# Optimization experiments

Hardware: AMD Instinct MI355X
Metric: run time of the kernel (lower is better)

Reference implementation:

```python
import jax, jax.numpy as jnp
import numpy as np


def setup_inputs() -> dict:
    key = jax.random.key(0)
    B, T, D, H = 32, 1600, 512, 512
    # variable lengths, nonincreasing (PackedSequence convention)
    lengths = np.array([T - 25 * i for i in range(B)])            # 1600 .. 825
    bs = (lengths[None, :] > np.arange(T)[:, None]).sum(1)        # batch_sizes[t], nonincreasing
    t_idx = np.repeat(np.arange(T), bs)                           # packed element -> timestep
    b_idx = np.concatenate([np.arange(b) for b in bs])            # packed element -> batch row
    mask = np.arange(B)[None, :] < bs[:, None]                    # [T,B] active mask
    total = int(bs.sum())                                         # 38800
    ks = jax.random.split(key, 7)
    s = 1.0 / np.sqrt(H)
    return {
        "packed_data": jax.random.normal(ks[0], (total, D), jnp.float32),
        "h0": jax.random.normal(ks[1], (B, H), jnp.float32),
        "c0": jax.random.normal(ks[2], (B, H), jnp.float32),
        "w_ih": jax.random.uniform(ks[3], (4 * H, D), jnp.float32, -s, s),
        "w_hh": jax.random.uniform(ks[4], (4 * H, H), jnp.float32, -s, s),
        "b_ih": jax.random.uniform(ks[5], (4 * H,), jnp.float32, -s, s),
        "b_hh": jax.random.uniform(ks[6], (4 * H,), jnp.float32, -s, s),
        "t_idx": jnp.asarray(t_idx, jnp.int32),
        "b_idx": jnp.asarray(b_idx, jnp.int32),
        "mask": jnp.asarray(mask),
    }


def reference(packed_data, h0, c0, w_ih, w_hh, b_ih, b_hh, t_idx, b_idx, mask):
    # Reverse LSTM over a packed variable-length batch.
    # Equivalent math to the torch loop: process timesteps T-1 .. 0; a row's
    # hidden stays at its initial value until the row becomes active.
    T, B = mask.shape
    D = packed_data.shape[1]
    # unpack to padded [T,B,D] (zeros at inactive slots; never read for output)
    padded = jnp.zeros((T, B, D), packed_data.dtype).at[t_idx, b_idx].set(packed_data)

    def step(carry, xm):
        h, c = carry
        x, m = xm                                   # x:[B,D], m:[B]
        gates = x @ w_ih.T + b_ih + h @ w_hh.T + b_hh   # [B,4H]
        i, f, g, o = jnp.split(gates, 4, axis=-1)
        c_new = jax.nn.sigmoid(f) * c + jax.nn.sigmoid(i) * jnp.tanh(g)
        h_new = jax.nn.sigmoid(o) * jnp.tanh(c_new)
        m2 = m[:, None]
        # inactive rows keep their initial hidden until they enter the batch
        return (jnp.where(m2, h_new, h0), jnp.where(m2, c_new, c0)), h_new

    (hT, cT), outs = jax.lax.scan(step, (h0, c0), (padded[::-1], mask[::-1]))
    outs = outs[::-1]                               # [T,B,H], time-forward order
    packed_out = outs[t_idx, b_idx]                 # repack [total,H]
    return packed_out, hT, cT
```

## Files before the change

### kernel.cpp

```cpp
#include <hip/hip_runtime.h>
#include <hip/hip_bf16.h>
#include <stdint.h>

typedef __attribute__((ext_vector_type(8))) short bf16x8;
typedef __attribute__((ext_vector_type(4))) float f32x4;
typedef __attribute__((ext_vector_type(4))) int int4v;
typedef unsigned long long u64;

#define DD 512
#define HH 512
#define BB 32

__device__ __forceinline__ unsigned short f2bf(float f) {
  unsigned u = __float_as_uint(f);
  u += 0x7fffu + ((u >> 16) & 1u);
  return (unsigned short)(u >> 16);
}
__device__ __forceinline__ int pk2(float a, float b) {
  return (int)((unsigned)f2bf(a) | ((unsigned)f2bf(b) << 16));
}
__device__ __forceinline__ float sigf(float x) { return 1.f / (1.f + __expf(-x)); }
__device__ __forceinline__ float tanhfast(float x) {
  float e = __expf(fminf(fmaxf(2.f * x, -60.f), 60.f));
  return (e - 1.f) / (e + 1.f);
}

__global__ void init_state(u64* hbuf, const float* __restrict__ h0, int* L) {
  int i = blockIdx.x * blockDim.x + threadIdx.x;
  if (i < 32) L[i] = 0;
  if (i < 16384) {
    int g = i >> 13, p = (i >> 12) & 1, m = (i >> 8) & 15, q = i & 255;
    u64 v;
    if (p == 0) {
      int b = g * 16 + m;
      unsigned lo = f2bf(h0[(size_t)b * HH + 2 * q]);
      unsigned hi = f2bf(h0[(size_t)b * HH + 2 * q + 1]);
      v = (u64)(lo | (hi << 16));
    } else {
      v = 0xFFFFFFFF00000000ull;
    }
    hbuf[i] = v;
  }
}

__global__ void init_idx(const int* __restrict__ t_idx, const int* __restrict__ b_idx,
                         int* rowstart, int* L, int total) {
  int r = blockIdx.x * blockDim.x + threadIdx.x;
  if (r >= total) return;
  int t = t_idx[r];
  if (r == 0 || t_idx[r - 1] != t) rowstart[t] = r;
  atomicMax(&L[b_idx[r]], t + 1);
}

__global__ __launch_bounds__(512, 2)
void lstm_main(const float* __restrict__ X, const float* __restrict__ h0,
               const float* __restrict__ c0, const float* __restrict__ w_ih,
               const float* __restrict__ w_hh, const float* __restrict__ b_ih,
               const float* __restrict__ b_hh, const int* __restrict__ rowstart,
               const int* __restrict__ L, u64* hbuf,
               float* out, int total)
{
  const int tid = threadIdx.x;
  const int bid = blockIdx.x;
  const int g = bid & 1;
  const int k = bid >> 1;
  const int lane = tid & 63;
  const int wave = tid >> 6;
  const int gate = wave & 3;
  const int cs = wave >> 2;
  const int ul = lane & 15;
  const int kc = lane >> 4;
  const int u0 = k * 32;
  const int j = gate * 512 + u0 + cs * 16 + ul;

  __shared__ unsigned short h_st[16 * DD];
  __shared__ unsigned short x_st[16 * DD];
  __shared__ float gl[4][16][32];

  bf16x8 wfa[16], wfb[16];
#pragma unroll
  for (int kk = 0; kk < 16; kk++) {
    const float* pa = w_ih + (size_t)j * DD + kk * 32 + kc * 8;
    const float* pb = w_hh + (size_t)j * DD + kk * 32 + kc * 8;
    bf16x8 va, vb;
#pragma unroll
    for (int e = 0; e < 8; e++) { va[e] = (short)f2bf(pa[e]); vb[e] = (short)f2bf(pb[e]); }
    wfa[kk] = va; wfb[kk] = vb;
  }
  const float bias = b_ih[j] + b_hh[j];

  const int mC = tid >> 5;
  const int uC = tid & 31;
  const int bcell = g * 16 + mC;
  const int Lc = L[bcell];
  float c_reg = c0[(size_t)bcell * HH + u0 + uC];
  const float c0c = c_reg;
  const float h0c = h0[(size_t)bcell * HH + u0 + uC];

  int t0 = 0;
#pragma unroll
  for (int m = 0; m < 16; m++) t0 = max(t0, L[g * 16 + m]);
  t0 -= 1;
  const int S = t0 + 1;

  u64* hb_g = hbuf + g * 8192;
  const size_t hT_off = (size_t)total * HH;
  const size_t cT_off = hT_off + (size_t)BB * HH;

  char* hst_c = (char*)h_st;
  char* xst_c = (char*)x_st;
  const int gr = (mC + k) & 15;
  const int gc = (uC + 2 * k) & 31;
  const int hbyte = gr * 1024 + gc * 32, hsw = (gr & 7) << 4;
  const int xbyte = mC * 1024 + uC * 32, xsw = (mC & 7) << 4;
  const int arow = ul * 1024, aswz = (ul & 7) << 4;

  f32x4 xr[4];
  {
    if (t0 < Lc) {
      const f32x4* xp = (const f32x4*)(X + (size_t)(rowstart[t0] + bcell) * DD + uC * 16);
#pragma unroll
      for (int q = 0; q < 4; q++) xr[q] = xp[q];
    } else {
#pragma unroll
      for (int q = 0; q < 4; q++) xr[q] = (f32x4){0.f, 0.f, 0.f, 0.f};
    }
  }

  for (int s = 0, t = t0; s < S; s++, t--) {
    const bool act = (t < Lc);
    {
      int4v e0 = {pk2(xr[0][0], xr[0][1]), pk2(xr[0][2], xr[0][3]),
                  pk2(xr[1][0], xr[1][1]), pk2(xr[1][2], xr[1][3])};
      int4v e1 = {pk2(xr[2][0], xr[2][1]), pk2(xr[2][2], xr[2][3]),
                  pk2(xr[3][0], xr[3][1]), pk2(xr[3][2], xr[3][3])};
      *(int4v*)(xst_c + (xbyte ^ xsw)) = e0;
      *(int4v*)(xst_c + ((xbyte + 16) ^ xsw)) = e1;
    }
    __syncthreads();

    const u64* src = hb_g + (size_t)((s & 1) * 4096) + gr * 256 + gc * 8;
    int4v c0v, c1v, c2v, c3v;
    asm volatile(
      "global_load_dwordx4 %0, %4, off sc0 sc1\n\t"
      "global_load_dwordx4 %1, %5, off sc0 sc1\n\t"
      "global_load_dwordx4 %2, %6, off sc0 sc1\n\t"
      "global_load_dwordx4 %3, %7, off sc0 sc1"
      : "=&v"(c0v), "=&v"(c1v), "=&v"(c2v), "=&v"(c3v)
      : "v"(src), "v"(src + 2), "v"(src + 4), "v"(src + 6)
      : "memory");

    f32x4 C = {bias, bias, bias, bias};
#pragma unroll
    for (int kk = 0; kk < 16; kk++) {
      bf16x8 A = *(const bf16x8*)(xst_c + ((arow + kk * 64 + kc * 16) ^ aswz));
      C = __builtin_amdgcn_mfma_f32_16x16x32_bf16(A, wfa[kk], C, 0, 0, 0);
    }

    asm volatile("s_waitcnt vmcnt(0)" ::: "memory");
    __builtin_amdgcn_sched_barrier(0);
    const unsigned want = (unsigned)s;
    int spins = 0;
    while (!(((unsigned)c0v[1] == want) & ((unsigned)c0v[3] == want) &
             ((unsigned)c1v[1] == want) & ((unsigned)c1v[3] == want) &
             ((unsigned)c2v[1] == want) & ((unsigned)c2v[3] == want) &
             ((unsigned)c3v[1] == want) & ((unsigned)c3v[3] == want))) {
      if (++spins < 4096) {
        asm volatile(
          "global_load_dwordx4 %0, %4, off sc0 sc1\n\t"
          "global_load_dwordx4 %1, %5, off sc0 sc1\n\t"
          "global_load_dwordx4 %2, %6, off sc0 sc1\n\t"
          "global_load_dwordx4 %3, %7, off sc0 sc1\n\t"
          "s_waitcnt vmcnt(0)"
          : "=&v"(c0v), "=&v"(c1v), "=&v"(c2v), "=&v"(c3v)
          : "v"(src), "v"(src + 2), "v"(src + 4), "v"(src + 6)
          : "memory");
        __builtin_amdgcn_sched_barrier(0);
      } else {
        u64 a0 = __hip_atomic_load(src + 0, __ATOMIC_RELAXED, __HIP_MEMORY_SCOPE_AGENT);
        u64 a1 = __hip_atomic_load(src + 1, __ATOMIC_RELAXED, __HIP_MEMORY_SCOPE_AGENT);
        u64 a2 = __hip_atomic_load(src + 2, __ATOMIC_RELAXED, __HIP_MEMORY_SCOPE_AGENT);
        u64 a3 = __hip_atomic_load(src + 3, __ATOMIC_RELAXED, __HIP_MEMORY_SCOPE_AGENT);
        u64 a4 = __hip_atomic_load(src + 4, __ATOMIC_RELAXED, __HIP_MEMORY_SCOPE_AGENT);
        u64 a5 = __hip_atomic_load(src + 5, __ATOMIC_RELAXED, __HIP_MEMORY_SCOPE_AGENT);
        u64 a6 = __hip_atomic_load(src + 6, __ATOMIC_RELAXED, __HIP_MEMORY_SCOPE_AGENT);
        u64 a7 = __hip_atomic_load(src + 7, __ATOMIC_RELAXED, __HIP_MEMORY_SCOPE_AGENT);
        c0v = (int4v){(int)a0, (int)(a0 >> 32), (int)a1, (int)(a1 >> 32)};
        c1v = (int4v){(int)a2, (int)(a2 >> 32), (int)a3, (int)(a3 >> 32)};
        c2v = (int4v){(int)a4, (int)(a4 >> 32), (int)a5, (int)(a5 >> 32)};
        c3v = (int4v){(int)a6, (int)(a6 >> 32), (int)a7, (int)(a7 >> 32)};
      }
    }

    {
      bool nact = false;
      if (t > 0) {
        nact = ((t - 1) < Lc);
        if (nact) {
          const f32x4* xp = (const f32x4*)(X + (size_t)(rowstart[t - 1] + bcell) * DD + uC * 16);
#pragma unroll
          for (int q = 0; q < 4; q++) xr[q] = xp[q];
        }
      }
      if (!nact) {
#pragma unroll
        for (int q = 0; q < 4; q++) xr[q] = (f32x4){0.f, 0.f, 0.f, 0.f};
      }
    }

    {
      int4v d0 = {c0v[0], c0v[2], c1v[0], c1v[2]};
      int4v d1 = {c2v[0], c2v[2], c3v[0], c3v[2]};
      *(int4v*)(hst_c + (hbyte ^ hsw)) = d0;
      *(int4v*)(hst_c + ((hbyte + 16) ^ hsw)) = d1;
    }
    __syncthreads();

    f32x4 C2 = {0.f, 0.f, 0.f, 0.f};
#pragma unroll
    for (int kk = 0; kk < 8; kk++) {
      bf16x8 A0 = *(const bf16x8*)(hst_c + ((arow + (2 * kk) * 64 + kc * 16) ^ aswz));
      bf16x8 A1 = *(const bf16x8*)(hst_c + ((arow + (2 * kk + 1) * 64 + kc * 16) ^ aswz));
      C  = __builtin_amdgcn_mfma_f32_16x16x32_bf16(A0, wfb[2 * kk], C, 0, 0, 0);
      C2 = __builtin_amdgcn_mfma_f32_16x16x32_bf16(A1, wfb[2 * kk + 1], C2, 0, 0, 0);
    }
#pragma unroll
    for (int r = 0; r < 4; r++) C[r] += C2[r];

#pragma unroll
    for (int r = 0; r < 4; r++) gl[gate][kc * 4 + r][cs * 16 + ul] = C[r];
    __syncthreads();

    float gi = gl[0][mC][uC], gf = gl[1][mC][uC], gg = gl[2][mC][uC], go = gl[3][mC][uC];
    float iv = sigf(gi), fv = sigf(gf), gv = tanhfast(gg), ov = sigf(go);
    float cn = fv * c_reg + iv * gv;
    float hn = ov * tanhfast(cn);
    float hp = act ? hn : h0c;
    c_reg = act ? cn : c0c;

    {
      unsigned hbf = (unsigned)f2bf(hp);
      unsigned v1 = __shfl_down(hbf, 1);
      if ((uC & 1) == 0) {
        u64 val = ((u64)(unsigned)(s + 1) << 32) | (hbf & 0xffffu) | ((v1 & 0xffffu) << 16);
        u64* dst = hb_g + (size_t)(((s + 1) & 1) * 4096) + mC * 256 + k * 16 + (uC >> 1);
        __hip_atomic_store(dst, val, __ATOMIC_RELAXED, __HIP_MEMORY_SCOPE_AGENT);
      }
    }

    if (act) {
      const int rst = rowstart[t];
      out[(size_t)(rst + bcell) * HH + u0 + uC] = hn;
      if (t == 0) {
        out[hT_off + (size_t)bcell * HH + u0 + uC] = hn;
        out[cT_off + (size_t)bcell * HH + u0 + uC] = cn;
      }
    }
  }
}

extern "C" void kernel_launch(void* const* d_in, const int* in_sizes, int n_in,
                              void* d_out, int out_size, void* d_ws, size_t ws_size,
                              hipStream_t stream) {
  const float* X    = (const float*)d_in[0];
  const float* h0   = (const float*)d_in[1];
  const float* c0   = (const float*)d_in[2];
  const float* w_ih = (const float*)d_in[3];
  const float* w_hh = (const float*)d_in[4];
  const float* b_ih = (const float*)d_in[5];
  const float* b_hh = (const float*)d_in[6];
  const int* t_idx  = (const int*)d_in[7];
  const int* b_idx  = (const int*)d_in[8];
  int total = in_sizes[0] / DD;

  u64* hbuf     = (u64*)d_ws;
  int* rowstart = (int*)((char*)d_ws + 131072);
  int* L        = rowstart + 2048;

  hipLaunchKernelGGL(init_state, dim3(64), dim3(256), 0, stream, hbuf, h0, L);
  hipLaunchKernelGGL(init_idx, dim3((total + 255) / 256), dim3(256), 0, stream,
                     t_idx, b_idx, rowstart, L, total);
  hipLaunchKernelGGL(lstm_main, dim3(32), dim3(512), 0, stream,
                     X, h0, c0, w_ih, w_hh, b_ih, b_hh, rowstart, L, hbuf,
                     (float*)d_out, total);
}
```

Measured before the change: 4.521 ms.

## Precompute input projection with a parallel GEMM before the recurrent loop

Adds a standalone bf16 MFMA GEMM that computes X·W_ih^T plus both biases for all packed rows up front and stores the result as bf16 in the workspace. The recurrent kernel then only does the h·W_hh product per step and adds the precomputed gate inputs, which removes the x staging, a barrier and 16 MFMAs from the serial critical path. It also splits the recurrent accumulation into two chains and pads the gate scratch array. The cost is an extra kernel plus about 160 MB of bf16 writes and reads, and extra rounding of the input contribution. The old fused kernel is kept as a fallback when the workspace is too small.

```diff
diff --git a/kernel.cpp b/kernel.cpp
--- a/kernel.cpp
+++ b/kernel.cpp
@@ -18,6 +18,9 @@
 }
 __device__ __forceinline__ int pk2(float a, float b) {
   return (int)((unsigned)f2bf(a) | ((unsigned)f2bf(b) << 16));
+}
+__device__ __forceinline__ float bf2f(unsigned short v) {
+  return __uint_as_float((unsigned)v << 16);
 }
 __device__ __forceinline__ float sigf(float x) { return 1.f / (1.f + __expf(-x)); }
 __device__ __forceinline__ float tanhfast(float x) {
@@ -52,13 +55,100 @@
   atomicMax(&L[b_idx[r]], t + 1);
 }
 
+__global__ __launch_bounds__(256, 2)
+void gx_gemm(const float* __restrict__ X, const float* __restrict__ w_ih,
+             const float* __restrict__ b_ih, const float* __restrict__ b_hh,
+             unsigned short* __restrict__ GX, int total)
+{
+  const int ct = blockIdx.x & 7;
+  const int rt = blockIdx.x >> 3;
+  const int r0 = rt * 64;
+  const int j0 = ct * 256;
+  const int tid = threadIdx.x;
+  const int lane = tid & 63, wv = tid >> 6;
+  const int ul = lane & 15, kc = lane >> 4;
+
+  __shared__ unsigned short As[64 * 64];
+  __shared__ unsigned short Bs[256 * 64];
+  char* As_c = (char*)As;
+  char* Bs_c = (char*)Bs;
+
+  f32x4 acc[4][4];
+#pragma unroll
+  for (int mf = 0; mf < 4; mf++)
+#pragma unroll
+    for (int nf = 0; nf < 4; nf++) acc[mf][nf] = (f32x4){0.f, 0.f, 0.f, 0.f};
+
+  const int arow_s = tid >> 2;
+  const int akq = (tid & 3) * 16;
+  const size_t arow_g = (size_t)min(r0 + arow_s, total - 1);
+  const int ab = arow_s * 128 + akq * 2, asw = (arow_s & 7) << 4;
+  const int bcol = tid;
+  const int bb = bcol * 128, bsw = (bcol & 7) << 4;
+
+  for (int ch = 0; ch < 8; ch++) {
+    const int k0 = ch * 64;
+    {
+      const f32x4* ap = (const f32x4*)(X + arow_g * DD + k0 + akq);
+      f32x4 a0 = ap[0], a1 = ap[1], a2 = ap[2], a3 = ap[3];
+      int4v p0 = {pk2(a0[0], a0[1]), pk2(a0[2], a0[3]), pk2(a1[0], a1[1]), pk2(a1[2], a1[3])};
+      int4v p1 = {pk2(a2[0], a2[1]), pk2(a2[2], a2[3]), pk2(a3[0], a3[1]), pk2(a3[2], a3[3])};
+      *(int4v*)(As_c + (ab ^ asw)) = p0;
+      *(int4v*)(As_c + ((ab + 16) ^ asw)) = p1;
+    }
+    {
+      const f32x4* bp = (const f32x4*)(w_ih + (size_t)(j0 + bcol) * DD + k0);
+#pragma unroll
+      for (int q = 0; q < 4; q++) {
+        f32x4 b0 = bp[4 * q], b1 = bp[4 * q + 1], b2 = bp[4 * q + 2], b3 = bp[4 * q + 3];
+        int4v p0 = {pk2(b0[0], b0[1]), pk2(b0[2], b0[3]), pk2(b1[0], b1[1]), pk2(b1[2], b1[3])};
+        int4v p1 = {pk2(b2[0], b2[1]), pk2(b2[2], b2[3]), pk2(b3[0], b3[1]), pk2(b3[2], b3[3])};
+        *(int4v*)(Bs_c + ((bb + q * 32) ^ bsw)) = p0;
+        *(int4v*)(Bs_c + ((bb + q * 32 + 16) ^ bsw)) = p1;
+      }
+    }
+    __syncthreads();
+#pragma unroll
+    for (int ks = 0; ks < 2; ks++) {
+      bf16x8 bfr[4], afr[4];
+#pragma unroll
+      for (int nf = 0; nf < 4; nf++) {
+        int col = wv * 64 + nf * 16 + ul;
+        bfr[nf] = *(const bf16x8*)(Bs_c + ((col * 128 + ks * 64 + kc * 16) ^ ((col & 7) << 4)));
+      }
+#pragma unroll
+      for (int mf = 0; mf < 4; mf++) {
+        int row = mf * 16 + ul;
+        afr[mf] = *(const bf16x8*)(As_c + ((row * 128 + ks * 64 + kc * 16) ^ ((row & 7) << 4)));
+      }
+#pragma unroll
+      for (int mf = 0; mf < 4; mf++)
+#pragma unroll
+        for (int nf = 0; nf < 4; nf++)
+          acc[mf][nf] = __builtin_amdgcn_mfma_f32_16x16x32_bf16(afr[mf], bfr[nf], acc[mf][nf], 0, 0, 0);
+    }
+    __syncthreads();
+  }
+#pragma unroll
+  for (int nf = 0; nf < 4; nf++) {
+    int c = j0 + wv * 64 + nf * 16 + ul;
+    float bias = b_ih[c] + b_hh[c];
+#pragma unroll
+    for (int mf = 0; mf < 4; mf++)
+#pragma unroll
+      for (int r = 0; r < 4; r++) {
+        int row = r0 + mf * 16 + kc * 4 + r;
+        if (row < total) GX[(size_t)row * 2048 + c] = f2bf(acc[mf][nf][r] + bias);
+      }
+  }
+}
+
 __global__ __launch_bounds__(512, 2)
-void lstm_main(const float* __restrict__ X, const float* __restrict__ h0,
-               const float* __restrict__ c0, const float* __restrict__ w_ih,
-               const float* __restrict__ w_hh, const float* __restrict__ b_ih,
-               const float* __restrict__ b_hh, const int* __restrict__ rowstart,
-               const int* __restrict__ L, u64* hbuf,
-               float* out, int total)
+void lstm_gx(const float* __restrict__ h0, const float* __restrict__ c0,
+             const float* __restrict__ w_hh,
+             const int* __restrict__ rowstart, const int* __restrict__ L,
+             u64* hbuf, const unsigned short* __restrict__ GX,
+             float* out, int total)
 {
   const int tid = threadIdx.x;
   const int bid = blockIdx.x;
@@ -73,29 +163,27 @@
   const int u0 = k * 32;
   const int j = gate * 512 + u0 + cs * 16 + ul;
 
-  __shared__ unsigned short h_st[16 * DD];
-  __shared__ unsigned short x_st[16 * DD];
-  __shared__ float gl[4][16][32];
-
-  bf16x8 wfa[16], wfb[16];
+  __shared__ unsigned short h_st[16 * HH];
+  __shared__ float gl[4][16][33];
+
+  bf16x8 wfb[16];
 #pragma unroll
   for (int kk = 0; kk < 16; kk++) {
-    const float* pa = w_ih + (size_t)j * DD + kk * 32 + kc * 8;
-    const float* pb = w_hh + (size_t)j * DD + kk * 32 + kc * 8;
-    bf16x8 va, vb;
-#pragma unroll
-    for (int e = 0; e < 8; e++) { va[e] = (short)f2bf(pa[e]); vb[e] = (short)f2bf(pb[e]); }
-    wfa[kk] = va; wfb[kk] = vb;
-  }
-  const float bias = b_ih[j] + b_hh[j];
+    const float* pb = w_hh + (size_t)j * HH + kk * 32 + kc * 8;
+    bf16x8 vb;
+#pragma unroll
+    for (int e = 0; e < 8; e++) vb[e] = (short)f2bf(pb[e]);
+    wfb[kk] = vb;
+  }
 
   const int mC = tid >> 5;
   const int uC = tid & 31;
   const int bcell = g * 16 + mC;
+  const int uu = u0 + uC;
   const int Lc = L[bcell];
-  float c_reg = c0[(size_t)bcell * HH + u0 + uC];
+  float c_reg = c0[(size_t)bcell * HH + uu];
   const float c0c = c_reg;
-  const float h0c = h0[(size_t)bcell * HH + u0 + uC];
+  const float h0c = h0[(size_t)bcell * HH + uu];
 
   int t0 = 0;
 #pragma unroll
@@ -108,37 +196,19 @@
   const size_t cT_off = hT_off + (size_t)BB * HH;
 
   char* hst_c = (char*)h_st;
-  char* xst_c = (char*)x_st;
   const int gr = (mC + k) & 15;
   const int gc = (uC + 2 * k) & 31;
   const int hbyte = gr * 1024 + gc * 32, hsw = (gr & 7) << 4;
-  const int xbyte = mC * 1024 + uC * 32, xsw = (mC & 7) << 4;
   const int arow = ul * 1024, aswz = (ul & 7) << 4;
 
-  f32x4 xr[4];
-  {
-    if (t0 < Lc) {
-      const f32x4* xp = (const f32x4*)(X + (size_t)(rowstart[t0] + bcell) * DD + uC * 16);
-#pragma unroll
-      for (int q = 0; q < 4; q++) xr[q] = xp[q];
-    } else {
-#pragma unroll
-      for (int q = 0; q < 4; q++) xr[q] = (f32x4){0.f, 0.f, 0.f, 0.f};
-    }
+  unsigned short gx0 = 0, gx1 = 0, gx2 = 0, gx3 = 0;
+  if (t0 < Lc) {
+    const unsigned short* gp = GX + (size_t)(rowstart[t0] + bcell) * 2048 + uu;
+    gx0 = gp[0]; gx1 = gp[512]; gx2 = gp[1024]; gx3 = gp[1536];
   }
 
   for (int s = 0, t = t0; s < S; s++, t--) {
     const bool act = (t < Lc);
-    {
-      int4v e0 = {pk2(xr[0][0], xr[0][1]), pk2(xr[0][2], xr[0][3]),
-                  pk2(xr[1][0], xr[1][1]), pk2(xr[1][2], xr[1][3])};
-      int4v e1 = {pk2(xr[2][0], xr[2][1]), pk2(xr[2][2], xr[2][3]),
-                  pk2(xr[3][0], xr[3][1]), pk2(xr[3][2], xr[3][3])};
-      *(int4v*)(xst_c + (xbyte ^ xsw)) = e0;
-      *(int4v*)(xst_c + ((xbyte + 16) ^ xsw)) = e1;
-    }
-    __syncthreads();
-
     const u64* src = hb_g + (size_t)((s & 1) * 4096) + gr * 256 + gc * 8;
     int4v c0v, c1v, c2v, c3v;
     asm volatile(
@@ -149,14 +219,6 @@
       : "=&v"(c0v), "=&v"(c1v), "=&v"(c2v), "=&v"(c3v)
       : "v"(src), "v"(src + 2), "v"(src + 4), "v"(src + 6)
       : "memory");
-
-    f32x4 C = {bias, bias, bias, bias};
-#pragma unroll
-    for (int kk = 0; kk < 16; kk++) {
-      bf16x8 A = *(const bf16x8*)(xst_c + ((arow + kk * 64 + kc * 16) ^ aswz));
-      C = __builtin_amdgcn_mfma_f32_16x16x32_bf16(A, wfa[kk], C, 0, 0, 0);
-    }
-
     asm volatile("s_waitcnt vmcnt(0)" ::: "memory");
     __builtin_amdgcn_sched_barrier(0);
     const unsigned want = (unsigned)s;
@@ -193,6 +255,203 @@
     }
 
     {
+      int4v d0 = {c0v[0], c0v[2], c1v[0], c1v[2]};
+      int4v d1 = {c2v[0], c2v[2], c3v[0], c3v[2]};
+      *(int4v*)(hst_c + (hbyte ^ hsw)) = d0;
+      *(int4v*)(hst_c + ((hbyte + 16) ^ hsw)) = d1;
+    }
+    unsigned short ngx0 = 0, ngx1 = 0, ngx2 = 0, ngx3 = 0;
+    if (t > 0 && (t - 1) < Lc) {
+      const unsigned short* gp = GX + (size_t)(rowstart[t - 1] + bcell) * 2048 + uu;
+      ngx0 = gp[0]; ngx1 = gp[512]; ngx2 = gp[1024]; ngx3 = gp[1536];
+    }
+    __syncthreads();
+
+    f32x4 C = {0.f, 0.f, 0.f, 0.f};
+    f32x4 C2 = {0.f, 0.f, 0.f, 0.f};
+#pragma unroll
+    for (int kk = 0; kk < 8; kk++) {
+      bf16x8 A0 = *(const bf16x8*)(hst_c + ((arow + (2 * kk) * 64 + kc * 16) ^ aswz));
+      bf16x8 A1 = *(const bf16x8*)(hst_c + ((arow + (2 * kk + 1) * 64 + kc * 16) ^ aswz));
+      C  = __builtin_amdgcn_mfma_f32_16x16x32_bf16(A0, wfb[2 * kk], C, 0, 0, 0);
+      C2 = __builtin_amdgcn_mfma_f32_16x16x32_bf16(A1, wfb[2 * kk + 1], C2, 0, 0, 0);
+    }
+#pragma unroll
+    for (int r = 0; r < 4; r++) gl[gate][kc * 4 + r][cs * 16 + ul] = C[r] + C2[r];
+    __syncthreads();
+
+    float gi = gl[0][mC][uC] + bf2f(gx0);
+    float gf = gl[1][mC][uC] + bf2f(gx1);
+    float gg = gl[2][mC][uC] + bf2f(gx2);
+    float go = gl[3][mC][uC] + bf2f(gx3);
+    float iv = sigf(gi), fv = sigf(gf), gv = tanhfast(gg), ov = sigf(go);
+    float cn = fv * c_reg + iv * gv;
+    float hn = ov * tanhfast(cn);
+    float hp = act ? hn : h0c;
+    c_reg = act ? cn : c0c;
+
+    {
+      unsigned hbf = (unsigned)f2bf(hp);
+      unsigned v1 = __shfl_down(hbf, 1);
+      if ((uC & 1) == 0) {
+        u64 val = ((u64)(unsigned)(s + 1) << 32) | (hbf & 0xffffu) | ((v1 & 0xffffu) << 16);
+        u64* dst = hb_g + (size_t)(((s + 1) & 1) * 4096) + mC * 256 + k * 16 + (uC >> 1);
+        __hip_atomic_store(dst, val, __ATOMIC_RELAXED, __HIP_MEMORY_SCOPE_AGENT);
+      }
+    }
+    if (act) {
+      const int rst = rowstart[t];
+      out[(size_t)(rst + bcell) * HH + uu] = hn;
+      if (t == 0) {
+        out[hT_off + (size_t)bcell * HH + uu] = hn;
+        out[cT_off + (size_t)bcell * HH + uu] = cn;
+      }
+    }
+    gx0 = ngx0; gx1 = ngx1; gx2 = ngx2; gx3 = ngx3;
+  }
+}
+
+__global__ __launch_bounds__(512, 2)
+void lstm_fused(const float* __restrict__ X, const float* __restrict__ h0,
+                const float* __restrict__ c0, const float* __restrict__ w_ih,
+                const float* __restrict__ w_hh, const float* __restrict__ b_ih,
+                const float* __restrict__ b_hh, const int* __restrict__ rowstart,
+                const int* __restrict__ L, u64* hbuf,
+                float* out, int total)
+{
+  const int tid = threadIdx.x;
+  const int bid = blockIdx.x;
+  const int g = bid & 1;
+  const int k = bid >> 1;
+  const int lane = tid & 63;
+  const int wave = tid >> 6;
+  const int gate = wave & 3;
+  const int cs = wave >> 2;
+  const int ul = lane & 15;
+  const int kc = lane >> 4;
+  const int u0 = k * 32;
+  const int j = gate * 512 + u0 + cs * 16 + ul;
+
+  __shared__ unsigned short h_st[16 * DD];
+  __shared__ unsigned short x_st[16 * DD];
+  __shared__ float gl[4][16][32];
+
+  bf16x8 wfa[16], wfb[16];
+#pragma unroll
+  for (int kk = 0; kk < 16; kk++) {
+    const float* pa = w_ih + (size_t)j * DD + kk * 32 + kc * 8;
+    const float* pb = w_hh + (size_t)j * DD + kk * 32 + kc * 8;
+    bf16x8 va, vb;
+#pragma unroll
+    for (int e = 0; e < 8; e++) { va[e] = (short)f2bf(pa[e]); vb[e] = (short)f2bf(pb[e]); }
+    wfa[kk] = va; wfb[kk] = vb;
+  }
+  const float bias = b_ih[j] + b_hh[j];
+
+  const int mC = tid >> 5;
+  const int uC = tid & 31;
+  const int bcell = g * 16 + mC;
+  const int Lc = L[bcell];
+  float c_reg = c0[(size_t)bcell * HH + u0 + uC];
+  const float c0c = c_reg;
+  const float h0c = h0[(size_t)bcell * HH + u0 + uC];
+
+  int t0 = 0;
+#pragma unroll
+  for (int m = 0; m < 16; m++) t0 = max(t0, L[g * 16 + m]);
+  t0 -= 1;
+  const int S = t0 + 1;
+
+  u64* hb_g = hbuf + g * 8192;
+  const size_t hT_off = (size_t)total * HH;
+  const size_t cT_off = hT_off + (size_t)BB * HH;
+
+  char* hst_c = (char*)h_st;
+  char* xst_c = (char*)x_st;
+  const int gr = (mC + k) & 15;
+  const int gc = (uC + 2 * k) & 31;
+  const int hbyte = gr * 1024 + gc * 32, hsw = (gr & 7) << 4;
+  const int xbyte = mC * 1024 + uC * 32, xsw = (mC & 7) << 4;
+  const int arow = ul * 1024, aswz = (ul & 7) << 4;
+
+  f32x4 xr[4];
+  {
+    if (t0 < Lc) {
+      const f32x4* xp = (const f32x4*)(X + (size_t)(rowstart[t0] + bcell) * DD + uC * 16);
+#pragma unroll
+      for (int q = 0; q < 4; q++) xr[q] = xp[q];
+    } else {
+#pragma unroll
+      for (int q = 0; q < 4; q++) xr[q] = (f32x4){0.f, 0.f, 0.f, 0.f};
+    }
+  }
+
+  for (int s = 0, t = t0; s < S; s++, t--) {
+    const bool act = (t < Lc);
+    {
+      int4v e0 = {pk2(xr[0][0], xr[0][1]), pk2(xr[0][2], xr[0][3]),
+                  pk2(xr[1][0], xr[1][1]), pk2(xr[1][2], xr[1][3])};
+      int4v e1 = {pk2(xr[2][0], xr[2][1]), pk2(xr[2][2], xr[2][3]),
+                  pk2(xr[3][0], xr[3][1]), pk2(xr[3][2], xr[3][3])};
+      *(int4v*)(xst_c + (xbyte ^ xsw)) = e0;
+      *(int4v*)(xst_c + ((xbyte + 16) ^ xsw)) = e1;
+    }
+    __syncthreads();
+
+    const u64* src = hb_g + (size_t)((s & 1) * 4096) + gr * 256 + gc * 8;
+    int4v c0v, c1v, c2v, c3v;
+    asm volatile(
+      "global_load_dwordx4 %0, %4, off sc0 sc1\n\t"
+      "global_load_dwordx4 %1, %5, off sc0 sc1\n\t"
+      "global_load_dwordx4 %2, %6, off sc0 sc1\n\t"
+      "global_load_dwordx4 %3, %7, off sc0 sc1"
+      : "=&v"(c0v), "=&v"(c1v), "=&v"(c2v), "=&v"(c3v)
+      : "v"(src), "v"(src + 2), "v"(src + 4), "v"(src + 6)
+      : "memory");
+
+    f32x4 C = {bias, bias, bias, bias};
+#pragma unroll
+    for (int kk = 0; kk < 16; kk++) {
+      bf16x8 A = *(const bf16x8*)(xst_c + ((arow + kk * 64 + kc * 16) ^ aswz));
+      C = __builtin_amdgcn_mfma_f32_16x16x32_bf16(A, wfa[kk], C, 0, 0, 0);
+    }
+
+    asm volatile("s_waitcnt vmcnt(0)" ::: "memory");
+    __builtin_amdgcn_sched_barrier(0);
+    const unsigned want = (unsigned)s;
+    int spins = 0;
+    while (!(((unsigned)c0v[1] == want) & ((unsigned)c0v[3] == want) &
+             ((unsigned)c1v[1] == want) & ((unsigned)c1v[3] == want) &
+             ((unsigned)c2v[1] == want) & ((unsigned)c2v[3] == want) &
+             ((unsigned)c3v[1] == want) & ((unsigned)c3v[3] == want))) {
+      if (++spins < 4096) {
+        asm volatile(
+          "global_load_dwordx4 %0, %4, off sc0 sc1\n\t"
+          "global_load_dwordx4 %1, %5, off sc0 sc1\n\t"
+          "global_load_dwordx4 %2, %6, off sc0 sc1\n\t"
+          "global_load_dwordx4 %3, %7, off sc0 sc1\n\t"
+          "s_waitcnt vmcnt(0)"
+          : "=&v"(c0v), "=&v"(c1v), "=&v"(c2v), "=&v"(c3v)
+          : "v"(src), "v"(src + 2), "v"(src + 4), "v"(src + 6)
+          : "memory");
+        __builtin_amdgcn_sched_barrier(0);
+      } else {
+        u64 a0 = __hip_atomic_load(src + 0, __ATOMIC_RELAXED, __HIP_MEMORY_SCOPE_AGENT);
+        u64 a1 = __hip_atomic_load(src + 1, __ATOMIC_RELAXED, __HIP_MEMORY_SCOPE_AGENT);
+        u64 a2 = __hip_atomic_load(src + 2, __ATOMIC_RELAXED, __HIP_MEMORY_SCOPE_AGENT);
+        u64 a3 = __hip_atomic_load(src + 3, __ATOMIC_RELAXED, __HIP_MEMORY_SCOPE_AGENT);
+        u64 a4 = __hip_atomic_load(src + 4, __ATOMIC_RELAXED, __HIP_MEMORY_SCOPE_AGENT);
+        u64 a5 = __hip_atomic_load(src + 5, __ATOMIC_RELAXED, __HIP_MEMORY_SCOPE_AGENT);
+        u64 a6 = __hip_atomic_load(src + 6, __ATOMIC_RELAXED, __HIP_MEMORY_SCOPE_AGENT);
+        u64 a7 = __hip_atomic_load(src + 7, __ATOMIC_RELAXED, __HIP_MEMORY_SCOPE_AGENT);
+        c0v = (int4v){(int)a0, (int)(a0 >> 32), (int)a1, (int)(a1 >> 32)};
+        c1v = (int4v){(int)a2, (int)(a2 >> 32), (int)a3, (int)(a3 >> 32)};
+        c2v = (int4v){(int)a4, (int)(a4 >> 32), (int)a5, (int)(a5 >> 32)};
+        c3v = (int4v){(int)a6, (int)(a6 >> 32), (int)a7, (int)(a7 >> 32)};
+      }
+    }
+
+    {
       bool nact = false;
       if (t > 0) {
         nact = ((t - 1) < Lc);
@@ -276,11 +535,22 @@
   u64* hbuf     = (u64*)d_ws;
   int* rowstart = (int*)((char*)d_ws + 131072);
   int* L        = rowstart + 2048;
+  const size_t GX_OFF = 147456;
+  unsigned short* GX = (unsigned short*)((char*)d_ws + GX_OFF);
+  const size_t need = GX_OFF + (size_t)total * 2048 * 2;
 
   hipLaunchKernelGGL(init_state, dim3(64), dim3(256), 0, stream, hbuf, h0, L);
   hipLaunchKernelGGL(init_idx, dim3((total + 255) / 256), dim3(256), 0, stream,
                      t_idx, b_idx, rowstart, L, total);
-  hipLaunchKernelGGL(lstm_main, dim3(32), dim3(512), 0, stream,
-                     X, h0, c0, w_ih, w_hh, b_ih, b_hh, rowstart, L, hbuf,
-                     (float*)d_out, total);
-}
+  if (ws_size >= need) {
+    int rt = (total + 63) >> 6;
+    hipLaunchKernelGGL(gx_gemm, dim3(rt * 8), dim3(256), 0, stream,
+                       X, w_ih, b_ih, b_hh, GX, total);
+    hipLaunchKernelGGL(lstm_gx, dim3(32), dim3(512), 0, stream,
+                       h0, c0, w_hh, rowstart, L, hbuf, GX, (float*)d_out, total);
+  } else {
+    hipLaunchKernelGGL(lstm_fused, dim3(32), dim3(512), 0, stream,
+                       X, h0, c0, w_ih, w_hh, b_ih, b_hh, rowstart, L, hbuf,
+                       (float*)d_out, total);
+  }
+}
```

Result: faster. 4.268 ms (median of 3 runs) (-5.6%).
